# Kernel optimization log

Measured on AMD Instinct MI355X. Metric: run time of the kernel, lower is better.

The kernel has to match this reference:

```python
import jax, jax.numpy as jnp
import numpy as np

B, L, D = 64, 4096, 256

def _make_perms():
    # Faithful to original: np.random.seed(i); np.random.permutation(arange(L)) per sample
    perms = np.empty((B, L), dtype=np.int32)
    mseq = np.arange(L)
    for i in range(B):
        np.random.seed(i)
        perms[i] = np.random.permutation(mseq)
    return jnp.asarray(perms)

def setup_inputs() -> dict:
    key = jax.random.key(0)
    x = jax.random.normal(key, (B, L, D), dtype=jnp.float32)
    perm = _make_perms()
    return {"x": x, "perm": perm}

def reference(x, perm):
    # Batched gather along the sequence axis: out[b, l, :] = x[b, perm[b, l], :]
    return jnp.take_along_axis(x, perm[:, :, None], axis=1)
```

## Files before the change

kernel.cpp:

```cpp
#include <hip/hip_runtime.h>


#define B_DIM 64
#define L_DIM 4096
#define D_DIM 256
#define D4    (D_DIM / 4)

__global__ __launch_bounds__(256) void gather_rows_kernel(
    const float4* __restrict__ x,
    const int*    __restrict__ perm,
    float4*       __restrict__ out)
{
    const int wave_in_block = threadIdx.x >> 6;
    const int lane          = threadIdx.x & 63;
    const int row           = blockIdx.x * 4 + wave_in_block;

    const int b = row >> 12;
    const int src = perm[row];

    const long out_off = (long)row * D4 + lane;
    const long in_off  = ((long)b * L_DIM + (long)src) * D4 + lane;

    out[out_off] = x[in_off];
}

extern "C" void kernel_launch(void* const* d_in, const int* in_sizes, int n_in,
                              void* d_out, int out_size, void* d_ws, size_t ws_size,
                              hipStream_t stream) {
    const float4* x    = (const float4*)d_in[0];
    const int*    perm = (const int*)d_in[1];
    float4*       out  = (float4*)d_out;

    const int total_rows = B_DIM * L_DIM;
    const int blocks     = total_rows / 4;

    gather_rows_kernel<<<blocks, 256, 0, stream>>>(x, perm, out);
}
```

Baseline: 420.1 us.

## Use persistent grid-stride gather with 8-way unrolled independent loads

```diff
diff --git a/kernel.cpp b/kernel.cpp
--- a/kernel.cpp
+++ b/kernel.cpp
@@ -1,27 +1,46 @@
 #include <hip/hip_runtime.h>
 
 
-#define B_DIM 64
-#define L_DIM 4096
-#define D_DIM 256
-#define D4    (D_DIM / 4)
+#define B_DIM   64
+#define L_DIM   4096
+#define D_DIM   256
+#define D4      (D_DIM / 4)
+#define TOTAL4  (B_DIM * L_DIM * D4)
+#define NBLK    2048
+#define NTHR    256
+#define UNROLL  8
 
-__global__ __launch_bounds__(256) void gather_rows_kernel(
+__global__ __launch_bounds__(NTHR) void gather_rows_kernel(
     const float4* __restrict__ x,
     const int*    __restrict__ perm,
     float4*       __restrict__ out)
 {
-    const int wave_in_block = threadIdx.x >> 6;
-    const int lane          = threadIdx.x & 63;
-    const int row           = blockIdx.x * 4 + wave_in_block;
+    const int tid    = blockIdx.x * NTHR + threadIdx.x;
+    const int stride = NBLK * NTHR;
 
-    const int b = row >> 12;
-    const int src = perm[row];
-
-    const long out_off = (long)row * D4 + lane;
-    const long in_off  = ((long)b * L_DIM + (long)src) * D4 + lane;
-
-    out[out_off] = x[in_off];
+    for (int base = tid; base < TOTAL4; base += stride * UNROLL) {
+        int src[UNROLL];
+        #pragma unroll
+        for (int u = 0; u < UNROLL; ++u) {
+            const int e   = base + u * stride;
+            const int row = e >> 6;
+            src[u] = perm[row];
+        }
+        float4 v[UNROLL];
+        #pragma unroll
+        for (int u = 0; u < UNROLL; ++u) {
+            const int e    = base + u * stride;
+            const int row  = e >> 6;
+            const int b    = row >> 12;
+            const int lane = e & 63;
+            const long in_off = ((long)(b << 12) + (long)src[u]) * D4 + lane;
+            v[u] = x[in_off];
+        }
+        #pragma unroll
+        for (int u = 0; u < UNROLL; ++u) {
+            out[base + u * stride] = v[u];
+        }
+    }
 }
 
 extern "C" void kernel_launch(void* const* d_in, const int* in_sizes, int n_in,
@@ -31,8 +50,5 @@
     const int*    perm = (const int*)d_in[1];
     float4*       out  = (float4*)d_out;
 
-    const int total_rows = B_DIM * L_DIM;
-    const int blocks     = total_rows / 4;
-
-    gather_rows_kernel<<<blocks, 256, 0, stream>>>(x, perm, out);
+    gather_rows_kernel<<<NBLK, NTHR, 0, stream>>>(x, perm, out);
 }
```

After: 448.1 us. 1.07x slower.

## Process 32 rows per wave with batched loads and shuffled perm indices

Applied to the files above, without the earlier changes.

```diff
diff --git a/kernel.cpp b/kernel.cpp
--- a/kernel.cpp
+++ b/kernel.cpp
@@ -1,27 +1,41 @@
 #include <hip/hip_runtime.h>
 
 
-#define B_DIM 64
-#define L_DIM 4096
-#define D_DIM 256
-#define D4    (D_DIM / 4)
+#define B_DIM  64
+#define L_DIM  4096
+#define D4     64
+#define NBLK   2048
+#define NTHR   256
+#define ROWS_PER_WAVE 32
 
-__global__ __launch_bounds__(256) void gather_rows_kernel(
+__global__ __launch_bounds__(NTHR) void gather_rows_kernel(
     const float4* __restrict__ x,
     const int*    __restrict__ perm,
     float4*       __restrict__ out)
 {
-    const int wave_in_block = threadIdx.x >> 6;
-    const int lane          = threadIdx.x & 63;
-    const int row           = blockIdx.x * 4 + wave_in_block;
+    const int wave  = (blockIdx.x * NTHR + threadIdx.x) >> 6;
+    const int lane  = threadIdx.x & 63;
+    const int wbase = wave * ROWS_PER_WAVE;
+    const int b     = wbase >> 12;
+    const long xb   = (long)b << 18;
 
-    const int b = row >> 12;
-    const int src = perm[row];
+    const int pv = perm[wbase + (lane & 31)];
 
-    const long out_off = (long)row * D4 + lane;
-    const long in_off  = ((long)b * L_DIM + (long)src) * D4 + lane;
+    #pragma unroll
+    for (int i = 0; i < ROWS_PER_WAVE; i += 4) {
+        int s[4];
+        #pragma unroll
+        for (int k = 0; k < 4; ++k) s[k] = __shfl(pv, i + k);
 
-    out[out_off] = x[in_off];
+        float4 v[4];
+        #pragma unroll
+        for (int k = 0; k < 4; ++k)
+            v[k] = x[xb + (long)s[k] * D4 + lane];
+
+        #pragma unroll
+        for (int k = 0; k < 4; ++k)
+            out[(long)(wbase + i + k) * D4 + lane] = v[k];
+    }
 }
 
 extern "C" void kernel_launch(void* const* d_in, const int* in_sizes, int n_in,
@@ -31,8 +45,5 @@
     const int*    perm = (const int*)d_in[1];
     float4*       out  = (float4*)d_out;
 
-    const int total_rows = B_DIM * L_DIM;
-    const int blocks     = total_rows / 4;
-
-    gather_rows_kernel<<<blocks, 256, 0, stream>>>(x, perm, out);
+    gather_rows_kernel<<<NBLK, NTHR, 0, stream>>>(x, perm, out);
 }
```

Measured after the change: 433.7 us. 1.03x slower.
